# Kernel optimization log

Measured on AMD Instinct MI355X. Metric: run time of the kernel, lower is better.

The kernel has to match this reference:

```python
import jax, jax.numpy as jnp
import numpy as np

B, T, E, H = 2, 2048, 1024, 16
HS = E // H  # head size 64


def setup_inputs() -> dict:
    key = jax.random.key(0)
    ks = jax.random.split(key, 6)
    s = 0.02
    return {
        "x": jax.random.normal(ks[0], (B, T, E), dtype=jnp.float32),
        "Wq": jax.random.normal(ks[1], (E, E), dtype=jnp.float32) * s,
        "Wk": jax.random.normal(ks[2], (E, E), dtype=jnp.float32) * s,
        "Wv": jax.random.normal(ks[3], (E, E), dtype=jnp.float32) * s,
        "Wp": jax.random.normal(ks[4], (E, E), dtype=jnp.float32) * s,
        "bp": jax.random.normal(ks[5], (E,), dtype=jnp.float32) * s,
    }


def reference(x, Wq, Wk, Wv, Wp, bp):
    b, t, e = x.shape
    # per-head projections (concatenated heads == single E->E matmul, reshaped)
    def heads(w):
        return jnp.einsum('bte,ef->btf', x, w).reshape(b, t, H, HS).transpose(0, 2, 1, 3)
    q, k, v = heads(Wq), heads(Wk), heads(Wv)  # [B,H,T,HS]
    # NOTE: original scales by full embed dim E, not head_size
    scores = jnp.einsum('bhqd,bhkd->bhqk', q, k) * (e ** -0.5)
    causal = jnp.tril(jnp.ones((t, t), dtype=bool))
    scores = jnp.where(causal, scores, -jnp.inf)
    probs = jax.nn.softmax(scores, axis=-1)
    # dropout is identity in eval mode
    out = jnp.einsum('bhqk,bhkd->bhqd', probs, v)  # [B,H,T,HS]
    out = out.transpose(0, 2, 1, 3).reshape(b, t, e)
    return jnp.einsum('bte,ef->btf', out, Wp) + bp
```

## Files before the change

kernel.cpp:

```cpp
#include <hip/hip_runtime.h>
#include <math.h>

typedef __bf16 bf16x8 __attribute__((ext_vector_type(8)));
typedef __bf16 bf16x4 __attribute__((ext_vector_type(4)));
typedef float f32x4 __attribute__((ext_vector_type(4)));

constexpr int Bb = 2, Tt = 2048, Ee = 1024, Hh = 16, Hs = 64;
constexpr int Mm = Bb * Tt;

__device__ inline unsigned short f2bf(float f) {
    union { float f; unsigned u; } c; c.f = f;
    unsigned u = c.u;
    u += 0x7FFFu + ((u >> 16) & 1u);
    return (unsigned short)(u >> 16);
}

#if __has_builtin(__builtin_amdgcn_exp2f)
#define EXP2(x) __builtin_amdgcn_exp2f(x)
#else
#define EXP2(x) exp2f(x)
#endif

__device__ inline void gl2lds16(const void* g, void* l) {
    __builtin_amdgcn_global_load_lds(
        (const __attribute__((address_space(1))) void*)g,
        (__attribute__((address_space(3))) void*)l, 16, 0, 0);
}

__device__ inline unsigned pk_bf16(float a, float b) {
    union { float f; unsigned u; } ca, cb;
    ca.f = a; cb.f = b;
    return __builtin_amdgcn_perm(ca.u + 0x8000u, cb.u + 0x8000u, 0x07060302u);
}

__global__ __launch_bounds__(256) void prep(const float* __restrict__ x,
                                            const float* __restrict__ Wq,
                                            const float* __restrict__ Wk,
                                            const float* __restrict__ Wv,
                                            const float* __restrict__ Wp,
                                            unsigned short* __restrict__ xb,
                                            unsigned short* __restrict__ wt3,
                                            unsigned short* __restrict__ wpt) {
    const int tid = threadIdx.x;
    if (blockIdx.z == 4) {
        int flat = (blockIdx.y * 16 + blockIdx.x) * 256 + tid;
#pragma unroll
        for (int i = 0; i < 16; i++) {
            int gid = flat + i * 65536;
            float4 v = ((const float4*)x)[gid];
            ushort4 o;
            o.x = f2bf(v.x); o.y = f2bf(v.y); o.z = f2bf(v.z); o.w = f2bf(v.w);
            ((ushort4*)xb)[gid] = o;
        }
        return;
    }
    __shared__ unsigned short t[64][68];
    const float* W = (blockIdx.z == 0) ? Wq : (blockIdx.z == 1) ? Wk
                    : (blockIdx.z == 2) ? Wv : Wp;
    unsigned short* dst = (blockIdx.z < 3) ? wt3 + (size_t)blockIdx.z * 1024 * 1024 : wpt;
    const int k0 = blockIdx.x * 64, n0 = blockIdx.y * 64;
#pragma unroll
    for (int j = 0; j < 4; j++) {
        int row = (tid >> 4) + j * 16;
        int c4 = (tid & 15) * 4;
        float4 v = *(const float4*)&W[(size_t)(k0 + row) * 1024 + n0 + c4];
        t[row][c4 + 0] = f2bf(v.x); t[row][c4 + 1] = f2bf(v.y);
        t[row][c4 + 2] = f2bf(v.z); t[row][c4 + 3] = f2bf(v.w);
    }
    __syncthreads();
#pragma unroll
    for (int j = 0; j < 16; j++) {
        int flat = j * 256 + tid;
        int orow = flat >> 6, ocol = flat & 63;
        dst[(size_t)(n0 + orow) * 1024 + k0 + ocol] = t[ocol][orow];
    }
}

__global__ __launch_bounds__(256, 3) void gemm_qkv(const unsigned short* __restrict__ A,
                                                   const unsigned short* __restrict__ Bt,
                                                   unsigned short* __restrict__ qb,
                                                   unsigned short* __restrict__ kb,
                                                   unsigned short* __restrict__ vtb) {
    __shared__ unsigned short As[128 * 64];
    __shared__ unsigned short Bs[128 * 64];
    const int tid = threadIdx.x;
    const int bid = blockIdx.x;
    const int swz = (bid & 7) * 96 + (bid >> 3);
    const int bx = swz % 24, by = swz / 24;
    const int bm = by * 128;
    const int bn = bx * 128;
    const int lane = tid & 63, w = tid >> 6;
    const int quad = lane >> 4, cl = lane & 15;
    const int wm = (w >> 1) * 64, wn = (w & 1) * 64;
    f32x4 acc[4][4] = {};

    auto stage = [&](int k0) {
#pragma unroll
        for (int i = 0; i < 4; i++) {
            int L = tid + i * 256;
            int r = L >> 3, s = L & 7;
            int c = s ^ (r & 7);
            gl2lds16(A + (size_t)(bm + r) * 1024 + k0 + c * 8, &As[L * 8]);
        }
#pragma unroll
        for (int i = 0; i < 4; i++) {
            int L = tid + i * 256;
            int r = L >> 3, s = L & 7;
            int c = s ^ (r & 7);
            gl2lds16(Bt + (size_t)(bn + r) * 1024 + k0 + c * 8, &Bs[L * 8]);
        }
    };

    stage(0);
    __syncthreads();
    for (int k0 = 0;;) {
#pragma unroll
        for (int kf = 0; kf < 2; kf++) {
            bf16x8 af[4], bfr[4];
            const int cc = kf * 4 + quad;
#pragma unroll
            for (int mt = 0; mt < 4; mt++) {
                int r = wm + mt * 16 + cl;
                af[mt] = *(const bf16x8*)&As[(r * 8 + (cc ^ (r & 7))) * 8];
                int rb = wn + mt * 16 + cl;
                bfr[mt] = *(const bf16x8*)&Bs[(rb * 8 + (cc ^ (rb & 7))) * 8];
            }
#pragma unroll
            for (int mt = 0; mt < 4; mt++)
#pragma unroll
                for (int nt = 0; nt < 4; nt++)
                    acc[mt][nt] = __builtin_amdgcn_mfma_f32_16x16x32_bf16(
                        af[mt], bfr[nt], acc[mt][nt], 0, 0, 0);
        }
        k0 += 64;
        if (k0 >= 1024) break;
        __syncthreads();
        stage(k0);
        __syncthreads();
    }

    const int region = bn >> 10;
    if (region < 2) {
        unsigned short* dst = region ? kb : qb;
        const float qs = region ? 1.0f : 0.045084220027780107f;
#pragma unroll
        for (int mt = 0; mt < 4; mt++)
#pragma unroll
            for (int nt = 0; nt < 4; nt++)
#pragma unroll
                for (int rg = 0; rg < 4; rg++) {
                    int m = bm + wm + mt * 16 + quad * 4 + rg;
                    int nn = (bn + wn + nt * 16 + cl) & 1023;
                    int b = m >> 11, t = m & 2047, h = nn >> 6, hs = nn & 63;
                    dst[((size_t)(b * 16 + h) * 2048 + t) * 64 + hs] =
                        f2bf(acc[mt][nt][rg] * qs);
                }
    } else {
#pragma unroll
        for (int mt = 0; mt < 4; mt++) {
            int m0 = bm + wm + mt * 16 + quad * 4;
            int b = m0 >> 11, t0 = m0 & 2047;
#pragma unroll
            for (int nt = 0; nt < 4; nt++) {
                int nn = (bn + wn + nt * 16 + cl) & 1023;
                int h = nn >> 6, hs = nn & 63;
                ushort4 pk;
                pk.x = f2bf(acc[mt][nt][0]); pk.y = f2bf(acc[mt][nt][1]);
                pk.z = f2bf(acc[mt][nt][2]); pk.w = f2bf(acc[mt][nt][3]);
                *(ushort4*)&vtb[((size_t)(b * 16 + h) * 64 + hs) * 2048 + t0] = pk;
            }
        }
    }
}

__global__ __launch_bounds__(256, 4) void gemm_out(const unsigned short* __restrict__ A,
                                                   const unsigned short* __restrict__ Bt,
                                                   const float* __restrict__ bias,
                                                   float* __restrict__ out) {
    __shared__ unsigned short As[64 * 64];
    __shared__ unsigned short Bs[128 * 64];
    const int tid = threadIdx.x;
    const int bid = blockIdx.x;
    const int swz = (bid & 7) * 64 + (bid >> 3);
    const int bx = swz & 7, by = swz >> 3;
    const int bm = by * 64;
    const int bn = bx * 128;
    const int lane = tid & 63, w = tid >> 6;
    const int quad = lane >> 4, cl = lane & 15;
    const int wm = (w >> 1) * 32, wn = (w & 1) * 64;
    f32x4 acc[2][4] = {};

    auto stage = [&](int k0) {
#pragma unroll
        for (int i = 0; i < 2; i++) {
            int L = tid + i * 256;
            int r = L >> 3, s = L & 7;
            int c = s ^ (r & 7);
            gl2lds16(A + (size_t)(bm + r) * 1024 + k0 + c * 8, &As[L * 8]);
        }
#pragma unroll
        for (int i = 0; i < 4; i++) {
            int L = tid + i * 256;
            int r = L >> 3, s = L & 7;
            int c = s ^ (r & 7);
            gl2lds16(Bt + (size_t)(bn + r) * 1024 + k0 + c * 8, &Bs[L * 8]);
        }
    };

    stage(0);
    __syncthreads();
    for (int k0 = 0;;) {
#pragma unroll
        for (int kf = 0; kf < 2; kf++) {
            bf16x8 af[2], bfr[4];
            const int cc = kf * 4 + quad;
#pragma unroll
            for (int mt = 0; mt < 2; mt++) {
                int r = wm + mt * 16 + cl;
                af[mt] = *(const bf16x8*)&As[(r * 8 + (cc ^ (r & 7))) * 8];
            }
#pragma unroll
            for (int nt = 0; nt < 4; nt++) {
                int rb = wn + nt * 16 + cl;
                bfr[nt] = *(const bf16x8*)&Bs[(rb * 8 + (cc ^ (rb & 7))) * 8];
            }
#pragma unroll
            for (int mt = 0; mt < 2; mt++)
#pragma unroll
                for (int nt = 0; nt < 4; nt++)
                    acc[mt][nt] = __builtin_amdgcn_mfma_f32_16x16x32_bf16(
                        af[mt], bfr[nt], acc[mt][nt], 0, 0, 0);
        }
        k0 += 64;
        if (k0 >= 1024) break;
        __syncthreads();
        stage(k0);
        __syncthreads();
    }

#pragma unroll
    for (int mt = 0; mt < 2; mt++)
#pragma unroll
        for (int nt = 0; nt < 4; nt++)
#pragma unroll
            for (int rg = 0; rg < 4; rg++) {
                int m = bm + wm + mt * 16 + quad * 4 + rg;
                int n = bn + wn + nt * 16 + cl;
                out[(size_t)m * 1024 + n] = acc[mt][nt][rg] + bias[n];
            }
}

__global__ __launch_bounds__(512, 2) void attn_mfma(const unsigned short* __restrict__ qg,
                                                    const unsigned short* __restrict__ kg,
                                                    const unsigned short* __restrict__ vtg,
                                                    unsigned short* __restrict__ og) {
    __shared__ unsigned short lds[32768];

    const int tid = threadIdx.x;
    const int idx = blockIdx.x;
    const int bh = idx & 31;
    const int j = idx >> 5;
    const int lane = tid & 63, w = tid >> 6;
    const int quad = lane >> 4, cl = lane & 15;
    const int g = w >> 2;
    const int qt = g ? (31 - j) : j;
    const int p = (w >> 1) & 1;
    const int qhalf = w & 1;
    const int qbase = qt * 64;
    const int qtL = 31 - j;
    const unsigned short* qB = qg + (size_t)bh * 2048 * 64;
    const unsigned short* kB = kg + (size_t)bh * 2048 * 64;
    const unsigned short* vB = vtg + (size_t)bh * 64 * 2048;

    float* Cmb = (float*)lds + g * 4608;
    float* Ll = Cmb + 4352;

    auto stageKV = [&](int kt) {
        unsigned short* Kd = lds + (kt & 3) * 4096;
        unsigned short* Vd = lds + 16384 + (kt & 3) * 4096;
        int L = tid;
        int r = L >> 3;
        int kc = (L & 7) ^ (r & 7);
        int grow = (r & 32) | ((r & 12) << 1) | ((r & 16) >> 2) | (r & 3);
        gl2lds16(kB + (size_t)(kt * 64 + grow) * 64 + kc * 8, &Kd[L * 8]);
        gl2lds16(vB + (size_t)r * 2048 + kt * 64 + kc * 8, &Vd[L * 8]);
    };

    bf16x8 qf[2][2];
#pragma unroll
    for (int nt2 = 0; nt2 < 2; nt2++)
#pragma unroll
        for (int kf = 0; kf < 2; kf++) {
            int row = qbase + qhalf * 32 + nt2 * 16 + cl;
            qf[nt2][kf] = *(const bf16x8*)&qB[(size_t)row * 64 + (kf * 4 + quad) * 8];
        }

    bf16x8 ones;
#pragma unroll
    for (int i = 0; i < 8; i++) ones[i] = (__bf16)1.0f;

    f32x4 oacc[2][4] = {};
    f32x4 lacc[2] = {};
    const int nit = (qtL + 2) >> 1;

    stageKV(0);
    stageKV(1);
    __syncthreads();

    for (int i = 0; i < nit; i++) {
        if (2 * i + 2 <= qtL) stageKV(2 * i + 2);
        if (2 * i + 3 <= qtL) stageKV(2 * i + 3);

        const int kt = 2 * i + p;
        if (kt <= qt) {
            const bool diag = (kt == qt);
            const unsigned short* Kl = lds + (kt & 3) * 4096;
            const unsigned short* Vl = lds + 16384 + (kt & 3) * 4096;
            f32x4 sac[4][2] = {};
            __builtin_amdgcn_s_setprio(1);
#pragma unroll
            for (int kf = 0; kf < 2; kf++)
#pragma unroll
                for (int mt = 0; mt < 4; mt++) {
                    int r = mt * 16 + cl, cc = kf * 4 + quad;
                    bf16x8 kf8 = *(const bf16x8*)&Kl[(r * 8 + (cc ^ (r & 7))) * 8];
#pragma unroll
                    for (int nt2 = 0; nt2 < 2; nt2++)
                        sac[mt][nt2] = __builtin_amdgcn_mfma_f32_16x16x32_bf16(
                            kf8, qf[nt2][kf], sac[mt][nt2], 0, 0, 0);
                }
            __builtin_amdgcn_s_setprio(0);
#pragma unroll
            for (int ks = 0; ks < 2; ks++) {
                bf16x8 pf[2];
#pragma unroll
                for (int nt2 = 0; nt2 < 2; nt2++) {
                    unsigned dw[4];
#pragma unroll
                    for (int mtl = 0; mtl < 2; mtl++) {
                        float pv[4];
#pragma unroll
                        for (int rg = 0; rg < 4; rg++) {
                            float e = EXP2(sac[ks * 2 + mtl][nt2][rg]);
                            if (diag && (ks * 32 + quad * 8 + mtl * 4 + rg >
                                         nt2 * 16 + cl + qhalf * 32))
                                e = 0.0f;
                            pv[rg] = e;
                        }
                        dw[mtl * 2 + 0] = pk_bf16(pv[1], pv[0]);
                        dw[mtl * 2 + 1] = pk_bf16(pv[3], pv[2]);
                    }
                    union { uint4 u; bf16x8 v; } cv;
                    cv.u = make_uint4(dw[0], dw[1], dw[2], dw[3]);
                    pf[nt2] = cv.v;
                }
                __builtin_amdgcn_s_setprio(1);
#pragma unroll
                for (int mt2 = 0; mt2 < 2; mt2++)
                    lacc[mt2] = __builtin_amdgcn_mfma_f32_16x16x32_bf16(
                        pf[mt2], ones, lacc[mt2], 0, 0, 0);
#pragma unroll
                for (int nt = 0; nt < 4; nt++) {
                    int r = nt * 16 + cl, cc = ks * 4 + quad;
                    bf16x8 vf = *(const bf16x8*)&Vl[(r * 8 + (cc ^ (r & 7))) * 8];
#pragma unroll
                    for (int mt2 = 0; mt2 < 2; mt2++)
                        oacc[mt2][nt] = __builtin_amdgcn_mfma_f32_16x16x32_bf16(
                            pf[mt2], vf, oacc[mt2][nt], 0, 0, 0);
                }
                __builtin_amdgcn_s_setprio(0);
            }
        }
        __syncthreads();
    }

    if (p == 1) {
#pragma unroll
        for (int mt2 = 0; mt2 < 2; mt2++)
#pragma unroll
            for (int rg = 0; rg < 4; rg++) {
                int row = qhalf * 32 + mt2 * 16 + quad * 4 + rg;
                if (cl == 0) Ll[row] = lacc[mt2][rg];
#pragma unroll
                for (int nt = 0; nt < 4; nt++)
                    Cmb[row * 68 + nt * 16 + cl] = oacc[mt2][nt][rg];
            }
    }
    __syncthreads();
    if (p == 0) {
        const int b = bh >> 4, h = bh & 15;
#pragma unroll
        for (int mt2 = 0; mt2 < 2; mt2++)
#pragma unroll
            for (int rg = 0; rg < 4; rg++) {
                int row = qhalf * 32 + mt2 * 16 + quad * 4 + rg;
                float inv = 1.0f / (lacc[mt2][rg] + Ll[row]);
                int t = qbase + row;
#pragma unroll
                for (int nt = 0; nt < 4; nt++) {
                    int hs = nt * 16 + cl;
                    float val = oacc[mt2][nt][rg] + Cmb[row * 68 + nt * 16 + cl];
                    og[((size_t)(b * 2048 + t)) * 1024 + h * 64 + hs] = f2bf(val * inv);
                }
            }
    }
}

extern "C" void kernel_launch(void* const* d_in, const int* in_sizes, int n_in,
                              void* d_out, int out_size, void* d_ws, size_t ws_size,
                              hipStream_t stream) {
    const float* x = (const float*)d_in[0];
    const float* Wq = (const float*)d_in[1];
    const float* Wk = (const float*)d_in[2];
    const float* Wv = (const float*)d_in[3];
    const float* Wp = (const float*)d_in[4];
    const float* bp = (const float*)d_in[5];
    float* out = (float*)d_out;

    unsigned short* xb = (unsigned short*)d_ws;
    unsigned short* wt3 = xb + (size_t)Mm * Ee;
    unsigned short* wpt = wt3 + (size_t)3 * Ee * Ee;
    unsigned short* qb = wpt + (size_t)Ee * Ee;
    unsigned short* kb = qb + (size_t)Mm * Ee;
    unsigned short* vtb = kb + (size_t)Mm * Ee;
    unsigned short* ab = vtb + (size_t)Mm * Ee;

    prep<<<dim3(16, 16, 5), dim3(256), 0, stream>>>(x, Wq, Wk, Wv, Wp, xb, wt3, wpt);
    gemm_qkv<<<dim3(768), dim3(256), 0, stream>>>(xb, wt3, qb, kb, vtb);
    attn_mfma<<<dim3(512), dim3(512), 0, stream>>>(qb, kb, vtb, ab);
    gemm_out<<<dim3(512), dim3(256), 0, stream>>>(ab, wpt, bp, out);
}
```

Baseline: 156.9 us.

## Restructure QKV GEMM into 256x192 double-buffered tiles with 512-thread blocks

The QKV projection GEMM now uses 256x192 output tiles computed by 8 waves (each 64x96), with double-buffered LDS and direct global-to-LDS prefetch of the next K slice overlapping the MFMA work on the current one. The grid becomes 16x16 blocks, exactly 256 workgroups to match the CU count. Raw waitcnt/barrier instructions and setprio wrap the MFMA section to cut synchronisation overhead. In exchange it uses more registers and about 112KB of LDS, giving one block per CU, and the epilogue has to handle a 192-wide tile that can straddle the q/k/v region boundaries.

```diff
diff --git a/kernel.cpp b/kernel.cpp
--- a/kernel.cpp
+++ b/kernel.cpp
@@ -32,6 +32,10 @@
     ca.f = a; cb.f = b;
     return __builtin_amdgcn_perm(ca.u + 0x8000u, cb.u + 0x8000u, 0x07060302u);
 }
+
+#define S_BARRIER() __builtin_amdgcn_s_barrier()
+#define WAIT_LGKM0() asm volatile("s_waitcnt lgkmcnt(0)" ::: "memory")
+#define WAIT_VM0() asm volatile("s_waitcnt vmcnt(0)" ::: "memory")
 
 __global__ __launch_bounds__(256) void prep(const float* __restrict__ x,
                                             const float* __restrict__ Wq,
@@ -76,98 +80,112 @@
     }
 }
 
-__global__ __launch_bounds__(256, 3) void gemm_qkv(const unsigned short* __restrict__ A,
+__global__ __launch_bounds__(512, 1) void gemm_qkv(const unsigned short* __restrict__ A,
                                                    const unsigned short* __restrict__ Bt,
                                                    unsigned short* __restrict__ qb,
                                                    unsigned short* __restrict__ kb,
                                                    unsigned short* __restrict__ vtb) {
-    __shared__ unsigned short As[128 * 64];
-    __shared__ unsigned short Bs[128 * 64];
+    __shared__ unsigned short As[2][16384];
+    __shared__ unsigned short Bs[2][12288];
     const int tid = threadIdx.x;
-    const int bid = blockIdx.x;
-    const int swz = (bid & 7) * 96 + (bid >> 3);
-    const int bx = swz % 24, by = swz / 24;
-    const int bm = by * 128;
-    const int bn = bx * 128;
+    const int bm = blockIdx.y * 256;
+    const int bn = blockIdx.x * 192;
     const int lane = tid & 63, w = tid >> 6;
     const int quad = lane >> 4, cl = lane & 15;
-    const int wm = (w >> 1) * 64, wn = (w & 1) * 64;
-    f32x4 acc[4][4] = {};
-
-    auto stage = [&](int k0) {
-#pragma unroll
-        for (int i = 0; i < 4; i++) {
-            int L = tid + i * 256;
-            int r = L >> 3, s = L & 7;
-            int c = s ^ (r & 7);
-            gl2lds16(A + (size_t)(bm + r) * 1024 + k0 + c * 8, &As[L * 8]);
-        }
-#pragma unroll
-        for (int i = 0; i < 4; i++) {
-            int L = tid + i * 256;
-            int r = L >> 3, s = L & 7;
-            int c = s ^ (r & 7);
-            gl2lds16(Bt + (size_t)(bn + r) * 1024 + k0 + c * 8, &Bs[L * 8]);
-        }
+    const int wm = (w >> 1) * 64;
+    const int wn = (w & 1) * 96;
+
+    f32x4 acc[4][6] = {};
+    bf16x8 a[4][2];
+    bf16x8 b[6][2];
+
+    const int sr = tid >> 3, ss = tid & 7;
+    const int sc = ss ^ (sr & 7);
+
+    auto stA = [&](int buf, int u, int kt) {
+        gl2lds16(A + (size_t)(bm + u * 64 + sr) * 1024 + kt * 64 + sc * 8,
+                 &As[buf][u * 4096 + tid * 8]);
     };
-
-    stage(0);
-    __syncthreads();
-    for (int k0 = 0;;) {
-#pragma unroll
-        for (int kf = 0; kf < 2; kf++) {
-            bf16x8 af[4], bfr[4];
-            const int cc = kf * 4 + quad;
-#pragma unroll
-            for (int mt = 0; mt < 4; mt++) {
-                int r = wm + mt * 16 + cl;
-                af[mt] = *(const bf16x8*)&As[(r * 8 + (cc ^ (r & 7))) * 8];
-                int rb = wn + mt * 16 + cl;
-                bfr[mt] = *(const bf16x8*)&Bs[(rb * 8 + (cc ^ (rb & 7))) * 8];
-            }
+    auto stB = [&](int buf, int u, int kt) {
+        gl2lds16(Bt + (size_t)(bn + u * 64 + sr) * 1024 + kt * 64 + sc * 8,
+                 &Bs[buf][u * 4096 + tid * 8]);
+    };
+    auto stageAll = [&](int buf, int kt) {
+        stB(buf, 0, kt); stB(buf, 1, kt); stB(buf, 2, kt);
+        stA(buf, 0, kt); stA(buf, 1, kt); stA(buf, 2, kt); stA(buf, 3, kt);
+    };
+
+    stageAll(0, 0);
+    WAIT_VM0();
+    S_BARRIER();
+
+    for (int t = 0; t < 16; ++t) {
+        const int cur = t & 1, nxt = cur ^ 1;
+        const bool pf = (t < 15);
+        if (pf) stageAll(nxt, t + 1);
+
+#pragma unroll
+        for (int mt = 0; mt < 4; mt++) {
+            int R = wm + mt * 16 + cl;
+#pragma unroll
+            for (int kf = 0; kf < 2; kf++) {
+                int cc = kf * 4 + quad;
+                a[mt][kf] = *(const bf16x8*)&As[cur][(R * 8 + (cc ^ (R & 7))) * 8];
+            }
+        }
+#pragma unroll
+        for (int nt = 0; nt < 6; nt++) {
+            int R = wn + nt * 16 + cl;
+#pragma unroll
+            for (int kf = 0; kf < 2; kf++) {
+                int cc = kf * 4 + quad;
+                b[nt][kf] = *(const bf16x8*)&Bs[cur][(R * 8 + (cc ^ (R & 7))) * 8];
+            }
+        }
+        WAIT_LGKM0();
+        __builtin_amdgcn_sched_barrier(0);
+        __builtin_amdgcn_s_setprio(1);
+#pragma unroll
+        for (int kf = 0; kf < 2; kf++)
 #pragma unroll
             for (int mt = 0; mt < 4; mt++)
 #pragma unroll
-                for (int nt = 0; nt < 4; nt++)
+                for (int nt = 0; nt < 6; nt++)
                     acc[mt][nt] = __builtin_amdgcn_mfma_f32_16x16x32_bf16(
-                        af[mt], bfr[nt], acc[mt][nt], 0, 0, 0);
-        }
-        k0 += 64;
-        if (k0 >= 1024) break;
-        __syncthreads();
-        stage(k0);
-        __syncthreads();
-    }
-
-    const int region = bn >> 10;
-    if (region < 2) {
-        unsigned short* dst = region ? kb : qb;
-        const float qs = region ? 1.0f : 0.045084220027780107f;
-#pragma unroll
-        for (int mt = 0; mt < 4; mt++)
-#pragma unroll
-            for (int nt = 0; nt < 4; nt++)
+                        a[mt][kf], b[nt][kf], acc[mt][nt], 0, 0, 0);
+        __builtin_amdgcn_s_setprio(0);
+
+        if (pf) WAIT_VM0();
+        S_BARRIER();
+    }
+
+#pragma unroll
+    for (int ni = 0; ni < 6; ni++) {
+        int ncol = bn + wn + ni * 16 + cl;
+        int region = (bn + wn + ni * 16) >> 10;
+        int nn = ncol & 1023;
+        int h = nn >> 6, hs = nn & 63;
+        if (region < 2) {
+            unsigned short* dst = region ? kb : qb;
+            const float qs = region ? 1.0f : 0.045084220027780107f;
+#pragma unroll
+            for (int mi = 0; mi < 4; mi++)
 #pragma unroll
                 for (int rg = 0; rg < 4; rg++) {
-                    int m = bm + wm + mt * 16 + quad * 4 + rg;
-                    int nn = (bn + wn + nt * 16 + cl) & 1023;
-                    int b = m >> 11, t = m & 2047, h = nn >> 6, hs = nn & 63;
-                    dst[((size_t)(b * 16 + h) * 2048 + t) * 64 + hs] =
-                        f2bf(acc[mt][nt][rg] * qs);
+                    int m = bm + wm + mi * 16 + quad * 4 + rg;
+                    int b2 = m >> 11, t = m & 2047;
+                    dst[((size_t)(b2 * 16 + h) * 2048 + t) * 64 + hs] =
+                        f2bf(acc[mi][ni][rg] * qs);
                 }
-    } else {
-#pragma unroll
-        for (int mt = 0; mt < 4; mt++) {
-            int m0 = bm + wm + mt * 16 + quad * 4;
-            int b = m0 >> 11, t0 = m0 & 2047;
-#pragma unroll
-            for (int nt = 0; nt < 4; nt++) {
-                int nn = (bn + wn + nt * 16 + cl) & 1023;
-                int h = nn >> 6, hs = nn & 63;
+        } else {
+#pragma unroll
+            for (int mi = 0; mi < 4; mi++) {
+                int m0 = bm + wm + mi * 16 + quad * 4;
+                int b2 = m0 >> 11, t0 = m0 & 2047;
                 ushort4 pk;
-                pk.x = f2bf(acc[mt][nt][0]); pk.y = f2bf(acc[mt][nt][1]);
-                pk.z = f2bf(acc[mt][nt][2]); pk.w = f2bf(acc[mt][nt][3]);
-                *(ushort4*)&vtb[((size_t)(b * 16 + h) * 64 + hs) * 2048 + t0] = pk;
+                pk.x = f2bf(acc[mi][ni][0]); pk.y = f2bf(acc[mi][ni][1]);
+                pk.z = f2bf(acc[mi][ni][2]); pk.w = f2bf(acc[mi][ni][3]);
+                *(ushort4*)&vtb[((size_t)(b2 * 16 + h) * 64 + hs) * 2048 + t0] = pk;
             }
         }
     }
@@ -426,7 +444,7 @@
     unsigned short* ab = vtb + (size_t)Mm * Ee;
 
     prep<<<dim3(16, 16, 5), dim3(256), 0, stream>>>(x, Wq, Wk, Wv, Wp, xb, wt3, wpt);
-    gemm_qkv<<<dim3(768), dim3(256), 0, stream>>>(xb, wt3, qb, kb, vtb);
+    gemm_qkv<<<dim3(16, 16), dim3(512), 0, stream>>>(xb, wt3, qb, kb, vtb);
     attn_mfma<<<dim3(512), dim3(512), 0, stream>>>(qb, kb, vtb, ab);
     gemm_out<<<dim3(512), dim3(256), 0, stream>>>(ab, wpt, bp, out);
 }
```

After: 158.4 us. Within noise of the previous version (+0.9%).
